# Optimization experiments

Measured on AMD Instinct MI355X. Metric: run time of the kernel, lower is better.

The kernel has to match this reference:

```python
import jax, jax.numpy as jnp
import numpy as np

N_NODES = 50000
N_EDGES = 800000
D = 128          # d_model
N_LAYER = 4
N_GRAPHS = 128
N_IDS = 256      # nn.Embedding(256, d_model)


def setup_inputs() -> dict:
    key = jax.random.key(0)
    ks = jax.random.split(key, 10)
    s = 0.02
    return {
        "position_feature": jax.random.normal(ks[0], (N_NODES, 3), dtype=jnp.float32),
        "id_feature": jax.random.randint(ks[1], (N_NODES,), 0, N_IDS),
        "edge_index": jax.random.randint(ks[2], (2, N_EDGES), 0, N_NODES),
        "batch": jnp.sort(jax.random.randint(ks[3], (N_NODES,), 0, N_GRAPHS)),
        "num_graphs": N_GRAPHS,
        "Wp": jax.random.normal(ks[4], (3, D), dtype=jnp.float32) * s,
        "bp": jnp.zeros((D,), jnp.float32),
        "id_emb": jax.random.normal(ks[5], (N_IDS, D), dtype=jnp.float32) * s,
        "Wn": jax.random.normal(ks[6], (2 * D, D), dtype=jnp.float32) * s,
        "bn": jnp.zeros((D,), jnp.float32),
        "conv_W": jax.random.normal(ks[7], (N_LAYER, D, D), dtype=jnp.float32) * s,
        "conv_b": jnp.zeros((N_LAYER, D), jnp.float32),
        "Wa": jax.random.normal(ks[8], ((1 + N_LAYER) * D, D), dtype=jnp.float32) * s,
        "ba": jnp.zeros((D,), jnp.float32),
    }


def _gcn(x, W, b, src, dst, norm, n):
    # PyG GCNConv: h = x @ W; out[dst] += norm(e) * h[src]; out += bias
    h = x @ W
    msg = h[src] * norm[:, None]
    return jax.ops.segment_sum(msg, dst, num_segments=n) + b


def reference(position_feature, id_feature, edge_index, batch, num_graphs,
              Wp, bp, id_emb, Wn, bn, conv_W, conv_b, Wa, ba):
    n = position_feature.shape[0]
    # GCN normalization with self-loops (shared across all layers)
    loops = jnp.arange(n)
    src = jnp.concatenate([edge_index[0], loops])
    dst = jnp.concatenate([edge_index[1], loops])
    deg = jax.ops.segment_sum(jnp.ones_like(src, dtype=position_feature.dtype), dst, num_segments=n)
    dinv = jnp.where(deg > 0, jax.lax.rsqrt(deg), 0.0)
    norm = dinv[src] * dinv[dst]  # [E + N]

    pos = jax.nn.relu(position_feature @ Wp + bp)       # [N, D]
    idf = jax.nn.relu(id_emb[id_feature])               # [N, D]
    x = jax.nn.relu(jnp.concatenate([pos, idf], axis=1) @ Wn + bn)  # [N, D]

    gs = [jax.ops.segment_max(x, batch, num_segments=num_graphs)]   # g_embed_0
    h = x
    for l in range(conv_W.shape[0]):
        h = jax.nn.relu(_gcn(h, conv_W[l], conv_b[l], src, dst, norm, n))
        gs.append(jax.ops.segment_max(h, batch, num_segments=num_graphs))

    g_embed = jnp.concatenate(gs, axis=1)  # [G, (1+n_layer)*D]
    return g_embed @ Wa + ba               # [G, D]
```

## Files before the change

### kernel.cpp

```cpp
#include <hip/hip_runtime.h>

#define N_NODES 50000
#define N_EDGES 800000
#define D 128
#define NLAYER 4
#define NGRAPH 128
#define GDIM (5 * D)
#define NBUCK 196
#define BCAP 4608

typedef __attribute__((ext_vector_type(8))) short bf16x8;
typedef __attribute__((ext_vector_type(4))) float f32x4;

__device__ __forceinline__ float b2f(unsigned short u) {
    return __uint_as_float(((unsigned)u) << 16);
}
__device__ __forceinline__ unsigned short f2b(float f) {
    unsigned u = __float_as_uint(f);
    unsigned r = (u + 0x7fffu + ((u >> 16) & 1u)) >> 16;
    return (unsigned short)r;
}


__global__ __launch_bounds__(256) void k_bucket(
    const int* __restrict__ esrc, const int* __restrict__ edst,
    int* __restrict__ cnt, int* __restrict__ bcnt_rel, int* __restrict__ ebuf) {
    __shared__ int hcnt[NBUCK];
    __shared__ int hbase[NBUCK];
    int t = threadIdx.x;
    for (int i = t; i < NBUCK; i += 256) hcnt[i] = 0;
    __syncthreads();
    int e0 = blockIdx.x * 2048 + t;
    int d[8], s[8];
#pragma unroll
    for (int i = 0; i < 8; ++i) {
        int e = e0 + i * 256;
        if (e < N_EDGES) {
            d[i] = edst[e];
            s[i] = esrc[e];
            atomicAdd(&cnt[d[i]], 1);
            atomicAdd(&hcnt[d[i] >> 8], 1);
        } else {
            d[i] = -1;
        }
    }
    __syncthreads();
    for (int i = t; i < NBUCK; i += 256) {
        int c = hcnt[i];
        hbase[i] = (c > 0) ? (i * BCAP + atomicAdd(&bcnt_rel[i], c)) : 0;
        hcnt[i] = 0;
    }
    __syncthreads();
#pragma unroll
    for (int i = 0; i < 8; ++i) {
        if (d[i] >= 0) {
            int b = d[i] >> 8;
            int p = atomicAdd(&hcnt[b], 1);
            int pos = hbase[b] + p;
            if (pos < (b + 1) * BCAP)
                ebuf[pos] = (s[i] & 0xffff) | ((d[i] & 255) << 16);
        }
    }
}


__global__ void k_scanA(const int* __restrict__ cnt, int* __restrict__ offs,
                        int* __restrict__ chunkSum) {
    __shared__ int lds[256];
    int tid = threadIdx.x;
    int base = blockIdx.x * 1024 + tid * 4;
    int v[4];
    int s = 0;
#pragma unroll
    for (int j = 0; j < 4; ++j) {
        int idx = base + j;
        v[j] = (idx < N_NODES) ? cnt[idx] : 0;
        s += v[j];
    }
    lds[tid] = s;
    __syncthreads();
    int t = s;
    for (int off = 1; off < 256; off <<= 1) {
        int add = (tid >= off) ? lds[tid - off] : 0;
        __syncthreads();
        t += add;
        lds[tid] = t;
        __syncthreads();
    }
    int run = t - s;
#pragma unroll
    for (int j = 0; j < 4; ++j) {
        int idx = base + j;
        if (idx < N_NODES) offs[idx] = run;
        run += v[j];
    }
    if (tid == 255) chunkSum[blockIdx.x] = t;
}

__global__ void k_scanB(const int* __restrict__ chunkSum, int* __restrict__ chunkOff,
                        int nc) {
    __shared__ int lds[64];
    int tid = threadIdx.x;
    int v = (tid < nc) ? chunkSum[tid] : 0;
    lds[tid] = v;
    __syncthreads();
    int t = v;
    for (int off = 1; off < 64; off <<= 1) {
        int add = (tid >= off) ? lds[tid - off] : 0;
        __syncthreads();
        t += add;
        lds[tid] = t;
        __syncthreads();
    }
    if (tid < nc) chunkOff[tid] = t - v;
}

__global__ void k_scanC(int* __restrict__ offs, const int* __restrict__ chunkOff,
                        const int* __restrict__ cnt, float* __restrict__ dinv,
                        const int* __restrict__ batch, int* __restrict__ hist2) {
    int i = blockIdx.x * 256 + threadIdx.x;
    if (i < N_NODES) {
        offs[i] += chunkOff[i >> 10];
        int c = cnt[i];
        dinv[i] = 1.f / sqrtf((float)(c + 1));
        atomicAdd(&hist2[batch[i] * 128 + min(c, 127)], 1);
    }
}

__global__ __launch_bounds__(1024) void k_scan16k(int* __restrict__ hist2) {
    __shared__ int lds[1024];
    int t = threadIdx.x;
    int v[16];
    int s = 0;
#pragma unroll
    for (int j = 0; j < 16; ++j) { v[j] = hist2[t * 16 + j]; s += v[j]; }
    lds[t] = s;
    __syncthreads();
    int tot = s;
    for (int off = 1; off < 1024; off <<= 1) {
        int add = (t >= off) ? lds[t - off] : 0;
        __syncthreads();
        tot += add;
        lds[t] = tot;
        __syncthreads();
    }
    int run = tot - s;
#pragma unroll
    for (int j = 0; j < 16; ++j) { hist2[t * 16 + j] = run; run += v[j]; }
}

__global__ void k_scatter(const int* __restrict__ cnt, const int* __restrict__ batch,
                          int* __restrict__ hist2, int* __restrict__ perm) {
    int i = blockIdx.x * 256 + threadIdx.x;
    if (i < N_NODES) {
        int key = batch[i] * 128 + min(cnt[i], 127);
        int p = atomicAdd(&hist2[key], 1);
        perm[p] = i;
    }
}

__global__ __launch_bounds__(256) void k_fillB(
    const int* __restrict__ ebuf, const int* __restrict__ bcnt_rel,
    const int* __restrict__ offs, const float* __restrict__ dinv,
    unsigned int* __restrict__ csrs) {
    __shared__ int loffs[256];
    __shared__ int lcnt[256];
    __shared__ float ldinv[256];
    int b = blockIdx.x, t = threadIdx.x;
    int nbase = b << 8;
    if (nbase + t < N_NODES) {
        loffs[t] = offs[nbase + t];
        ldinv[t] = dinv[nbase + t];
    }
    lcnt[t] = 0;
    __syncthreads();
    int s0 = b * BCAP, s1 = b * BCAP + bcnt_rel[b];
    for (int i = s0 + t; i < s1; i += 256) {
        int pk = ebuf[i];
        int ld = (pk >> 16) & 255;
        int src = pk & 0xffff;
        float w = dinv[src] * ldinv[ld];
        int p = atomicAdd(&lcnt[ld], 1);
        csrs[loffs[ld] + p] = (unsigned)src | ((unsigned)f2b(w) << 16);
    }
}


__global__ __launch_bounds__(256) void k_prep(
    const float* __restrict__ Wn, const float* __restrict__ convW,
    unsigned short* __restrict__ Wpack,
    const float* __restrict__ id_emb, float* __restrict__ T) {
    int blk = blockIdx.x;
    if (blk < 320) {
        int tid = blk * 256 + threadIdx.x;
        int m = tid >> 14;
        int rem = tid & 16383;
        int ct = rem >> 11, kc = (rem >> 9) & 3, l = (rem >> 3) & 63, j = rem & 7;
        int k = kc * 32 + ((l >> 4) * 8) + j;
        int n = ct * 16 + (l & 15);
        const float* src = (m == 0) ? Wn : (convW + (size_t)(m - 1) * 16384);
        Wpack[tid] = f2b(src[k * 128 + n]);
    } else {
        int t = threadIdx.x;
        int d = t & 127;
        int r = (blk - 320) * 2 + (t >> 7);
        float acc = 0.f;
        for (int k = 0; k < 128; ++k)
            acc = fmaf(fmaxf(id_emb[r * 128 + k], 0.f), Wn[(128 + k) * 128 + d], acc);
        T[r * 128 + d] = acc;
    }
}


__global__ __launch_bounds__(256) void k_encoder(
    const float* __restrict__ pos, const int* __restrict__ idfeat,
    const float* __restrict__ Wp, const float* __restrict__ bp,
    const unsigned short* __restrict__ WpackE, const float* __restrict__ bn,
    const float* __restrict__ T, unsigned short* __restrict__ A16,
    const int* __restrict__ batch, float* __restrict__ gbuf) {
    __shared__ unsigned short feat[64 * 128];
    __shared__ float posl[192];
    __shared__ int bbat[64];
    int t = threadIdx.x;
    int base = blockIdx.x * 64;
    int avail = N_NODES - base;
    if (t < 192) {
        int idx = base * 3 + t;
        posl[t] = (idx < N_NODES * 3) ? pos[idx] : 0.f;
    }
    if (t < 64) bbat[t] = (base + t < N_NODES) ? batch[base + t] : -1;
    __syncthreads();
#pragma unroll
    for (int i = 0; i < 4; ++i) {
        int gid = t + i * 256;
        int row = gid >> 4, kg = gid & 15;
        unsigned short u[8];
        if (row < avail) {
            float p0 = posl[row * 3], p1 = posl[row * 3 + 1], p2 = posl[row * 3 + 2];
#pragma unroll
            for (int j = 0; j < 8; ++j) {
                int d = kg * 8 + j;
                float v = fmaf(p0, Wp[d], fmaf(p1, Wp[128 + d], fmaf(p2, Wp[256 + d], bp[d])));
                u[j] = f2b(fmaxf(v, 0.f));
            }
        } else {
#pragma unroll
            for (int j = 0; j < 8; ++j) u[j] = 0;
        }
        char* dst = (char*)feat + row * 256 + ((kg * 16) ^ ((row & 7) << 4));
        *(uint4*)dst = *(uint4*)u;
    }
    __syncthreads();
    int wid = t >> 6, l = t & 63;
    int r0 = wid * 16;
    f32x4 acc[8];
#pragma unroll
    for (int ct = 0; ct < 8; ++ct) acc[ct] = (f32x4){0.f, 0.f, 0.f, 0.f};
    const bf16x8* wp = (const bf16x8*)WpackE;
#pragma unroll
    for (int kc = 0; kc < 4; ++kc) {
        int row = r0 + (l & 15);
        const char* ap = (const char*)feat + row * 256 +
                         ((kc * 64 + ((l >> 4) * 16)) ^ ((row & 7) << 4));
        bf16x8 afrag = *(const bf16x8*)ap;
#pragma unroll
        for (int ct = 0; ct < 8; ++ct) {
            bf16x8 bfrag = wp[(ct * 4 + kc) * 64 + l];
            acc[ct] = __builtin_amdgcn_mfma_f32_16x16x32_bf16(afrag, bfrag, acc[ct], 0, 0, 0);
        }
    }
    int subrow = (l >> 4) * 4, col0 = l & 15;
    int ids[4];
#pragma unroll
    for (int i = 0; i < 4; ++i) {
        int node = base + r0 + subrow + i;
        ids[i] = (node < N_NODES) ? idfeat[node] : 0;
    }
    __syncthreads();
#pragma unroll
    for (int ct = 0; ct < 8; ++ct) {
        int col = ct * 16 + col0;
        float bcol = bn[col];
#pragma unroll
        for (int i = 0; i < 4; ++i) {
            int node = base + r0 + subrow + i;
            unsigned short ob = 0;
            if (node < N_NODES) {
                float v = acc[ct][i] + bcol + T[ids[i] * 128 + col];
                ob = f2b(fmaxf(v, 0.f));
                A16[(size_t)node * 128 + col] = ob;
            }
            feat[(r0 + subrow + i) * 128 + col] = ob;
        }
    }
    __syncthreads();
    if (t < 128) {
        int j = 0;
        while (j < 64) {
            int g = bbat[j];
            float m = b2f(feat[j * 128 + t]);
            int k = j + 1;
            while (k < 64 && bbat[k] == g) { m = fmaxf(m, b2f(feat[k * 128 + t])); ++k; }
            if (g >= 0) atomicMax((int*)&gbuf[g * GDIM + t], __float_as_int(m));
            j = k;
        }
    }
}


__global__ __launch_bounds__(256) void k_layer(
    const unsigned short* __restrict__ Hin, unsigned short* __restrict__ Hout,
    const unsigned short* __restrict__ WpackL,
    const int* __restrict__ offs, const int* __restrict__ cnt,
    const unsigned int* __restrict__ csrs, const float* __restrict__ dinv,
    const float* __restrict__ bias, const int* __restrict__ batch,
    const int* __restrict__ perm, float* __restrict__ gbuf, int goff) {
    __shared__ unsigned short hagg[16 * 128];
    __shared__ float smx[16][132];
    __shared__ int bb[16];
    __shared__ int snode[16];
    int tid = threadIdx.x;
    int wave = tid >> 6, lane = tid & 63;
    int q = lane >> 4, l16 = lane & 15;
    int row = wave * 4 + q;
    int nbase = blockIdx.x * 16;
    if (tid < 16) {
        int n = perm[nbase + tid];
        snode[tid] = n;
        bb[tid] = batch[n];
    }
    int node = perm[nbase + row];

    int start = offs[node];
    int c = cnt[node];
    float di = dinv[node];
    float sw = di * di;
    const uint4* B4 = (const uint4*)Hin;
    float a[8];
    {
        uint4 sv = B4[(size_t)node * 16 + l16];
        a[0] = sw * __uint_as_float(sv.x << 16);
        a[1] = sw * __uint_as_float(sv.x & 0xffff0000u);
        a[2] = sw * __uint_as_float(sv.y << 16);
        a[3] = sw * __uint_as_float(sv.y & 0xffff0000u);
        a[4] = sw * __uint_as_float(sv.z << 16);
        a[5] = sw * __uint_as_float(sv.z & 0xffff0000u);
        a[6] = sw * __uint_as_float(sv.w << 16);
        a[7] = sw * __uint_as_float(sv.w & 0xffff0000u);
    }
    int j = 0;
    for (; j + 8 <= c; j += 8) {
        unsigned pk[8];
        uint4 v[8];
#pragma unroll
        for (int i = 0; i < 8; ++i) pk[i] = csrs[start + j + i];
#pragma unroll
        for (int i = 0; i < 8; ++i) v[i] = B4[(size_t)(pk[i] & 0xffffu) * 16 + l16];
#pragma unroll
        for (int i = 0; i < 8; ++i) {
            float w = __uint_as_float(pk[i] & 0xffff0000u);
            a[0] = fmaf(w, __uint_as_float(v[i].x << 16), a[0]);
            a[1] = fmaf(w, __uint_as_float(v[i].x & 0xffff0000u), a[1]);
            a[2] = fmaf(w, __uint_as_float(v[i].y << 16), a[2]);
            a[3] = fmaf(w, __uint_as_float(v[i].y & 0xffff0000u), a[3]);
            a[4] = fmaf(w, __uint_as_float(v[i].z << 16), a[4]);
            a[5] = fmaf(w, __uint_as_float(v[i].z & 0xffff0000u), a[5]);
            a[6] = fmaf(w, __uint_as_float(v[i].w << 16), a[6]);
            a[7] = fmaf(w, __uint_as_float(v[i].w & 0xffff0000u), a[7]);
        }
    }
    for (; j < c; ++j) {
        unsigned pk = csrs[start + j];
        float w = __uint_as_float(pk & 0xffff0000u);
        uint4 v = B4[(size_t)(pk & 0xffffu) * 16 + l16];
        a[0] = fmaf(w, __uint_as_float(v.x << 16), a[0]);
        a[1] = fmaf(w, __uint_as_float(v.x & 0xffff0000u), a[1]);
        a[2] = fmaf(w, __uint_as_float(v.y << 16), a[2]);
        a[3] = fmaf(w, __uint_as_float(v.y & 0xffff0000u), a[3]);
        a[4] = fmaf(w, __uint_as_float(v.z << 16), a[4]);
        a[5] = fmaf(w, __uint_as_float(v.z & 0xffff0000u), a[5]);
        a[6] = fmaf(w, __uint_as_float(v.w << 16), a[6]);
        a[7] = fmaf(w, __uint_as_float(v.w & 0xffff0000u), a[7]);
    }
    {
        unsigned u[4];
#pragma unroll
        for (int k = 0; k < 4; ++k)
            u[k] = (unsigned)f2b(a[2 * k]) | ((unsigned)f2b(a[2 * k + 1]) << 16);
        char* dst = (char*)hagg + row * 256 + ((l16 * 16) ^ ((row & 7) << 4));
        *(uint4*)dst = *(uint4*)u;
    }
    __syncthreads();

    f32x4 oacc[2] = {(f32x4){0.f, 0.f, 0.f, 0.f}, (f32x4){0.f, 0.f, 0.f, 0.f}};
    const bf16x8* wp = (const bf16x8*)WpackL;
#pragma unroll
    for (int kc = 0; kc < 4; ++kc) {
        int arow = lane & 15;
        const char* ap = (const char*)hagg + arow * 256 +
                         ((kc * 64 + ((lane >> 4) * 16)) ^ ((arow & 7) << 4));
        bf16x8 afrag = *(const bf16x8*)ap;
#pragma unroll
        for (int ci = 0; ci < 2; ++ci) {
            int ct = wave * 2 + ci;
            bf16x8 bfrag = wp[(ct * 4 + kc) * 64 + lane];
            oacc[ci] = __builtin_amdgcn_mfma_f32_16x16x32_bf16(afrag, bfrag, oacc[ci], 0, 0, 0);
        }
    }

    int subrow = (lane >> 4) * 4;
#pragma unroll
    for (int ci = 0; ci < 2; ++ci) {
        int col = (wave * 2 + ci) * 16 + (lane & 15);
        float bcol = bias[col];
#pragma unroll
        for (int i = 0; i < 4; ++i) {
            int r = subrow + i;
            float v = fmaxf(oacc[ci][i] + bcol, 0.f);
            smx[r][col] = v;
            Hout[(size_t)snode[r] * 128 + col] = f2b(v);
        }
    }
    __syncthreads();
    if (tid < 128) {
        int jj = 0;
        while (jj < 16) {
            int g = bb[jj];
            float m = smx[jj][tid];
            int k = jj + 1;
            while (k < 16 && bb[k] == g) { m = fmaxf(m, smx[k][tid]); ++k; }
            atomicMax((int*)&gbuf[g * GDIM + goff + tid], __float_as_int(m));
            jj = k;
        }
    }
}


__global__ __launch_bounds__(128) void k_final(const float* __restrict__ gbuf,
                                               const float* __restrict__ Wa,
                                               const float* __restrict__ ba,
                                               float* __restrict__ out) {
    __shared__ float gr[GDIM];
    int g = blockIdx.x, t = threadIdx.x;
    for (int i = t; i < GDIM; i += 128) gr[i] = gbuf[g * GDIM + i];
    __syncthreads();
    float acc = ba[t];
    for (int k = 0; k < GDIM; ++k) acc = fmaf(gr[k], Wa[k * 128 + t], acc);
    out[g * 128 + t] = acc;
}


extern "C" void kernel_launch(void* const* d_in, const int* in_sizes, int n_in,
                              void* d_out, int out_size, void* d_ws, size_t ws_size,
                              hipStream_t stream) {
    const float* pos    = (const float*)d_in[0];
    const int*   idfeat = (const int*)d_in[1];
    const int*   eidx   = (const int*)d_in[2];
    const int*   batch  = (const int*)d_in[3];
    const float* Wp     = (const float*)d_in[5];
    const float* bp     = (const float*)d_in[6];
    const float* id_emb = (const float*)d_in[7];
    const float* Wn     = (const float*)d_in[8];
    const float* bn     = (const float*)d_in[9];
    const float* convW  = (const float*)d_in[10];
    const float* convb  = (const float*)d_in[11];
    const float* Wa     = (const float*)d_in[12];
    const float* ba     = (const float*)d_in[13];
    float* out = (float*)d_out;

    const int* esrc = eidx;
    const int* edst = eidx + N_EDGES;

    char* w = (char*)d_ws;
    auto alloc = [&](size_t bytes) -> char* {
        char* p = w;
        w += (bytes + 255) & ~(size_t)255;
        return p;
    };
    char* zstart = w;
    int*   cnt      = (int*)alloc((size_t)N_NODES * 4);
    float* gbuf     = (float*)alloc((size_t)NGRAPH * GDIM * 4);
    int*   hist2    = (int*)alloc((size_t)16384 * 4);
    int*   bcnt_rel = (int*)alloc((size_t)NBUCK * 4);
    size_t zbytes = (size_t)(w - zstart);

    unsigned short* A16a = (unsigned short*)alloc((size_t)N_NODES * D * 2);
    unsigned short* A16b = (unsigned short*)alloc((size_t)N_NODES * D * 2);
    float* dinv = (float*)alloc((size_t)N_NODES * 4);
    int*   offs = (int*)alloc((size_t)(N_NODES + 1) * 4);
    int*   csum = (int*)alloc(64 * 4);
    int*   coff = (int*)alloc(64 * 4);
    unsigned int* csrs = (unsigned int*)alloc((size_t)N_EDGES * 4);
    int*   ebuf = (int*)alloc((size_t)NBUCK * BCAP * 4);
    int*   perm = (int*)alloc((size_t)N_NODES * 4);
    float* T    = (float*)alloc((size_t)256 * D * 4);
    unsigned short* Wpack = (unsigned short*)alloc((size_t)5 * 16384 * 2);

    hipMemsetAsync(zstart, 0, zbytes, stream);

    k_bucket<<<(N_EDGES + 2047) / 2048, 256, 0, stream>>>(esrc, edst, cnt, bcnt_rel, ebuf);

    int nchunk = (N_NODES + 1023) / 1024;
    k_scanA<<<nchunk, 256, 0, stream>>>(cnt, offs, csum);
    k_scanB<<<1, 64, 0, stream>>>(csum, coff, nchunk);
    k_scanC<<<(N_NODES + 255) / 256, 256, 0, stream>>>(offs, coff, cnt, dinv, batch, hist2);
    k_scan16k<<<1, 1024, 0, stream>>>(hist2);
    k_scatter<<<(N_NODES + 255) / 256, 256, 0, stream>>>(cnt, batch, hist2, perm);

    k_fillB<<<NBUCK, 256, 0, stream>>>(ebuf, bcnt_rel, offs, dinv, csrs);

    k_prep<<<448, 256, 0, stream>>>(Wn, convW, Wpack, id_emb, T);
    k_encoder<<<(N_NODES + 63) / 64, 256, 0, stream>>>(pos, idfeat, Wp, bp, Wpack, bn, T,
                                                       A16a, batch, gbuf);

    unsigned short* Hin = A16a;
    unsigned short* Hout = A16b;
    for (int l = 0; l < NLAYER; ++l) {
        k_layer<<<N_NODES / 16, 256, 0, stream>>>(Hin, Hout, Wpack + (size_t)(l + 1) * 16384,
                                                  offs, cnt, csrs, dinv,
                                                  convb + (size_t)l * D, batch, perm, gbuf,
                                                  (l + 1) * D);
        unsigned short* tmp = Hin; Hin = Hout; Hout = tmp;
    }

    k_final<<<NGRAPH, 128, 0, stream>>>(gbuf, Wa, ba, out);
}
```

Before: 281.1 us.

## Derive degrees and CSR offsets from per-bucket LDS histograms instead of global atomics

Drops the global per-node atomic degree counting in the bucketing kernel. Each bucket block now computes node degrees with an LDS histogram, and offsets come from a small bucket-level scan plus an in-block scan. This replaces the three-kernel global scan with two lighter kernels and removes 800k global atomics. The cost is an extra read pass over the edge buffer, and the bucketing kernel now uses half the edges per block and twice as many blocks.

```diff
diff --git a/kernel.cpp b/kernel.cpp
--- a/kernel.cpp
+++ b/kernel.cpp
@@ -24,21 +24,20 @@
 
 __global__ __launch_bounds__(256) void k_bucket(
     const int* __restrict__ esrc, const int* __restrict__ edst,
-    int* __restrict__ cnt, int* __restrict__ bcnt_rel, int* __restrict__ ebuf) {
+    int* __restrict__ bcnt_rel, int* __restrict__ ebuf) {
     __shared__ int hcnt[NBUCK];
     __shared__ int hbase[NBUCK];
     int t = threadIdx.x;
     for (int i = t; i < NBUCK; i += 256) hcnt[i] = 0;
     __syncthreads();
-    int e0 = blockIdx.x * 2048 + t;
-    int d[8], s[8];
-#pragma unroll
-    for (int i = 0; i < 8; ++i) {
+    int e0 = blockIdx.x * 1024 + t;
+    int d[4], s[4];
+#pragma unroll
+    for (int i = 0; i < 4; ++i) {
         int e = e0 + i * 256;
         if (e < N_EDGES) {
             d[i] = edst[e];
             s[i] = esrc[e];
-            atomicAdd(&cnt[d[i]], 1);
             atomicAdd(&hcnt[d[i] >> 8], 1);
         } else {
             d[i] = -1;
@@ -52,7 +51,7 @@
     }
     __syncthreads();
 #pragma unroll
-    for (int i = 0; i < 8; ++i) {
+    for (int i = 0; i < 4; ++i) {
         if (d[i] >= 0) {
             int b = d[i] >> 8;
             int p = atomicAdd(&hcnt[b], 1);
@@ -64,102 +63,60 @@
 }
 
 
-__global__ void k_scanA(const int* __restrict__ cnt, int* __restrict__ offs,
-                        int* __restrict__ chunkSum) {
+__global__ void k_bscan(const int* __restrict__ bcnt_rel, int* __restrict__ bbase) {
     __shared__ int lds[256];
-    int tid = threadIdx.x;
-    int base = blockIdx.x * 1024 + tid * 4;
-    int v[4];
-    int s = 0;
-#pragma unroll
-    for (int j = 0; j < 4; ++j) {
-        int idx = base + j;
-        v[j] = (idx < N_NODES) ? cnt[idx] : 0;
-        s += v[j];
-    }
-    lds[tid] = s;
-    __syncthreads();
-    int t = s;
+    int t = threadIdx.x;
+    int v = (t < NBUCK) ? bcnt_rel[t] : 0;
+    lds[t] = v;
+    __syncthreads();
+    int tot = v;
     for (int off = 1; off < 256; off <<= 1) {
-        int add = (tid >= off) ? lds[tid - off] : 0;
-        __syncthreads();
-        t += add;
-        lds[tid] = t;
-        __syncthreads();
-    }
-    int run = t - s;
-#pragma unroll
-    for (int j = 0; j < 4; ++j) {
-        int idx = base + j;
-        if (idx < N_NODES) offs[idx] = run;
-        run += v[j];
-    }
-    if (tid == 255) chunkSum[blockIdx.x] = t;
-}
-
-__global__ void k_scanB(const int* __restrict__ chunkSum, int* __restrict__ chunkOff,
-                        int nc) {
-    __shared__ int lds[64];
-    int tid = threadIdx.x;
-    int v = (tid < nc) ? chunkSum[tid] : 0;
-    lds[tid] = v;
-    __syncthreads();
-    int t = v;
-    for (int off = 1; off < 64; off <<= 1) {
-        int add = (tid >= off) ? lds[tid - off] : 0;
-        __syncthreads();
-        t += add;
-        lds[tid] = t;
-        __syncthreads();
-    }
-    if (tid < nc) chunkOff[tid] = t - v;
-}
-
-__global__ void k_scanC(int* __restrict__ offs, const int* __restrict__ chunkOff,
-                        const int* __restrict__ cnt, float* __restrict__ dinv,
-                        const int* __restrict__ batch, int* __restrict__ hist2) {
-    int i = blockIdx.x * 256 + threadIdx.x;
-    if (i < N_NODES) {
-        offs[i] += chunkOff[i >> 10];
-        int c = cnt[i];
-        dinv[i] = 1.f / sqrtf((float)(c + 1));
-        atomicAdd(&hist2[batch[i] * 128 + min(c, 127)], 1);
-    }
-}
-
-__global__ __launch_bounds__(1024) void k_scan16k(int* __restrict__ hist2) {
-    __shared__ int lds[1024];
-    int t = threadIdx.x;
-    int v[16];
-    int s = 0;
-#pragma unroll
-    for (int j = 0; j < 16; ++j) { v[j] = hist2[t * 16 + j]; s += v[j]; }
-    lds[t] = s;
-    __syncthreads();
-    int tot = s;
-    for (int off = 1; off < 1024; off <<= 1) {
         int add = (t >= off) ? lds[t - off] : 0;
         __syncthreads();
         tot += add;
         lds[t] = tot;
         __syncthreads();
     }
-    int run = tot - s;
-#pragma unroll
-    for (int j = 0; j < 16; ++j) { hist2[t * 16 + j] = run; run += v[j]; }
-}
-
-__global__ void k_scatter(const int* __restrict__ cnt, const int* __restrict__ batch,
-                          int* __restrict__ hist2, int* __restrict__ perm) {
-    int i = blockIdx.x * 256 + threadIdx.x;
-    if (i < N_NODES) {
-        int key = batch[i] * 128 + min(cnt[i], 127);
-        int p = atomicAdd(&hist2[key], 1);
-        perm[p] = i;
-    }
-}
-
-__global__ __launch_bounds__(256) void k_fillB(
+    if (t < NBUCK) bbase[t] = tot - v;
+}
+
+
+__global__ __launch_bounds__(256) void k_fillB1(
+    const int* __restrict__ ebuf, const int* __restrict__ bcnt_rel,
+    const int* __restrict__ bbase, const int* __restrict__ batch,
+    int* __restrict__ offs, int* __restrict__ cnt, float* __restrict__ dinv,
+    int* __restrict__ hist2) {
+    __shared__ int lcnt[256];
+    __shared__ int lscan[256];
+    int b = blockIdx.x, t = threadIdx.x;
+    lcnt[t] = 0;
+    __syncthreads();
+    int s0 = b * BCAP, s1 = b * BCAP + bcnt_rel[b];
+    for (int i = s0 + t; i < s1; i += 256)
+        atomicAdd(&lcnt[(ebuf[i] >> 16) & 255], 1);
+    __syncthreads();
+    int v = lcnt[t];
+    lscan[t] = v;
+    __syncthreads();
+    int tot = v;
+    for (int off = 1; off < 256; off <<= 1) {
+        int add = (t >= off) ? lscan[t - off] : 0;
+        __syncthreads();
+        tot += add;
+        lscan[t] = tot;
+        __syncthreads();
+    }
+    int node = (b << 8) + t;
+    if (node < N_NODES) {
+        offs[node] = bbase[b] + (tot - v);
+        cnt[node] = v;
+        dinv[node] = 1.f / sqrtf((float)(v + 1));
+        atomicAdd(&hist2[batch[node] * 128 + min(v, 127)], 1);
+    }
+}
+
+
+__global__ __launch_bounds__(256) void k_fillB2(
     const int* __restrict__ ebuf, const int* __restrict__ bcnt_rel,
     const int* __restrict__ offs, const float* __restrict__ dinv,
     unsigned int* __restrict__ csrs) {
@@ -182,6 +139,38 @@
         float w = dinv[src] * ldinv[ld];
         int p = atomicAdd(&lcnt[ld], 1);
         csrs[loffs[ld] + p] = (unsigned)src | ((unsigned)f2b(w) << 16);
+    }
+}
+
+__global__ __launch_bounds__(1024) void k_scan16k(int* __restrict__ hist2) {
+    __shared__ int lds[1024];
+    int t = threadIdx.x;
+    int v[16];
+    int s = 0;
+#pragma unroll
+    for (int j = 0; j < 16; ++j) { v[j] = hist2[t * 16 + j]; s += v[j]; }
+    lds[t] = s;
+    __syncthreads();
+    int tot = s;
+    for (int off = 1; off < 1024; off <<= 1) {
+        int add = (t >= off) ? lds[t - off] : 0;
+        __syncthreads();
+        tot += add;
+        lds[t] = tot;
+        __syncthreads();
+    }
+    int run = tot - s;
+#pragma unroll
+    for (int j = 0; j < 16; ++j) { hist2[t * 16 + j] = run; run += v[j]; }
+}
+
+__global__ void k_scatter(const int* __restrict__ cnt, const int* __restrict__ batch,
+                          int* __restrict__ hist2, int* __restrict__ perm) {
+    int i = blockIdx.x * 256 + threadIdx.x;
+    if (i < N_NODES) {
+        int key = batch[i] * 128 + min(cnt[i], 127);
+        int p = atomicAdd(&hist2[key], 1);
+        perm[p] = i;
     }
 }
 
@@ -478,18 +467,17 @@
         return p;
     };
     char* zstart = w;
-    int*   cnt      = (int*)alloc((size_t)N_NODES * 4);
     float* gbuf     = (float*)alloc((size_t)NGRAPH * GDIM * 4);
     int*   hist2    = (int*)alloc((size_t)16384 * 4);
     int*   bcnt_rel = (int*)alloc((size_t)NBUCK * 4);
     size_t zbytes = (size_t)(w - zstart);
 
+    int*   cnt  = (int*)alloc((size_t)N_NODES * 4);
     unsigned short* A16a = (unsigned short*)alloc((size_t)N_NODES * D * 2);
     unsigned short* A16b = (unsigned short*)alloc((size_t)N_NODES * D * 2);
     float* dinv = (float*)alloc((size_t)N_NODES * 4);
     int*   offs = (int*)alloc((size_t)(N_NODES + 1) * 4);
-    int*   csum = (int*)alloc(64 * 4);
-    int*   coff = (int*)alloc(64 * 4);
+    int*   bbase= (int*)alloc((NBUCK + 1) * 4);
     unsigned int* csrs = (unsigned int*)alloc((size_t)N_EDGES * 4);
     int*   ebuf = (int*)alloc((size_t)NBUCK * BCAP * 4);
     int*   perm = (int*)alloc((size_t)N_NODES * 4);
@@ -498,16 +486,12 @@
 
     hipMemsetAsync(zstart, 0, zbytes, stream);
 
-    k_bucket<<<(N_EDGES + 2047) / 2048, 256, 0, stream>>>(esrc, edst, cnt, bcnt_rel, ebuf);
-
-    int nchunk = (N_NODES + 1023) / 1024;
-    k_scanA<<<nchunk, 256, 0, stream>>>(cnt, offs, csum);
-    k_scanB<<<1, 64, 0, stream>>>(csum, coff, nchunk);
-    k_scanC<<<(N_NODES + 255) / 256, 256, 0, stream>>>(offs, coff, cnt, dinv, batch, hist2);
+    k_bucket<<<(N_EDGES + 1023) / 1024, 256, 0, stream>>>(esrc, edst, bcnt_rel, ebuf);
+    k_bscan<<<1, 256, 0, stream>>>(bcnt_rel, bbase);
+    k_fillB1<<<NBUCK, 256, 0, stream>>>(ebuf, bcnt_rel, bbase, batch, offs, cnt, dinv, hist2);
     k_scan16k<<<1, 1024, 0, stream>>>(hist2);
     k_scatter<<<(N_NODES + 255) / 256, 256, 0, stream>>>(cnt, batch, hist2, perm);
-
-    k_fillB<<<NBUCK, 256, 0, stream>>>(ebuf, bcnt_rel, offs, dinv, csrs);
+    k_fillB2<<<NBUCK, 256, 0, stream>>>(ebuf, bcnt_rel, offs, dinv, csrs);
 
     k_prep<<<448, 256, 0, stream>>>(Wn, convW, Wpack, id_emb, T);
     k_encoder<<<(N_NODES + 63) / 64, 256, 0, stream>>>(pos, idfeat, Wp, bp, Wpack, bn, T,
```

Measured after the change: 260.7 us. 1.08x faster.
